# Kernel tuning notes

Measured on AMD Instinct MI355X. Metric: run time of the kernel, lower is better.

Reference implementation:

```python
import jax, jax.numpy as jnp
import numpy as np
from jax import lax

DIM = 64


def _dwconv(x, w, b):
    # x: [B,C,H,W], w: [C,1,kh,kw] depthwise, 'same' padding
    kh, kw = w.shape[2], w.shape[3]
    y = lax.conv_general_dilated(
        x, w, window_strides=(1, 1),
        padding=[(kh // 2, kh // 2), (kw // 2, kw // 2)],
        dimension_numbers=("NCHW", "OIHW", "NCHW"),
        feature_group_count=x.shape[1])
    return y + b[None, :, None, None]


def _conv1x1(x, w, b):
    y = lax.conv_general_dilated(
        x, w, window_strides=(1, 1), padding="VALID",
        dimension_numbers=("NCHW", "OIHW", "NCHW"))
    return y + b[None, :, None, None]


def _avgpool3(x):
    # PyTorch AvgPool2d(3,1,1) default count_include_pad=True -> sum/9
    s = lax.reduce_window(x, 0.0, lax.add, (1, 1, 3, 3), (1, 1, 1, 1),
                          [(0, 0), (0, 0), (1, 1), (1, 1)])
    return s / 9.0


def _maxpool3(x):
    return lax.reduce_window(x, -jnp.inf, lax.max, (1, 1, 3, 3), (1, 1, 1, 1),
                             [(0, 0), (0, 0), (1, 1), (1, 1)])


def setup_inputs() -> dict:
    key = jax.random.key(0)
    ks = jax.random.split(key, 18)
    C = DIM
    def w(k, shape):
        fan_in = shape[1] * shape[2] * shape[3]
        bound = 1.0 / np.sqrt(fan_in)
        return jax.random.uniform(k, shape, jnp.float32, -bound, bound)
    def b(k, fan_in):
        bound = 1.0 / np.sqrt(fan_in)
        return jax.random.uniform(k, (C,), jnp.float32, -bound, bound)
    return {
        "x": jax.random.normal(ks[0], (16, C, 128, 128), jnp.float32),
        "w55": w(ks[1], (C, 1, 5, 5)), "b55": b(ks[2], 25),
        "w17_0": w(ks[3], (C, 1, 1, 7)), "b17_0": b(ks[4], 7),
        "w17_1": w(ks[5], (C, 1, 7, 1)), "b17_1": b(ks[6], 7),
        "w111_0": w(ks[7], (C, 1, 1, 11)), "b111_0": b(ks[8], 11),
        "w111_1": w(ks[9], (C, 1, 11, 1)), "b111_1": b(ks[10], 11),
        "w211_0": w(ks[11], (C, 1, 1, 21)), "b211_0": b(ks[12], 21),
        "w211_1": w(ks[13], (C, 1, 21, 1)), "b211_1": b(ks[14], 21),
        "w11": w(ks[15], (C, C, 1, 1)), "b11": b(ks[16], C),
    }


def reference(x, w55, b55, w17_0, b17_0, w17_1, b17_1,
              w111_0, b111_0, w111_1, b111_1,
              w211_0, b211_0, w211_1, b211_1, w11, b11):
    def branch(inp):
        c55 = _dwconv(inp, w55, b55)
        c17 = _dwconv(_dwconv(inp, w17_0, b17_0), w17_1, b17_1)
        c111 = _dwconv(_dwconv(inp, w111_0, b111_0), w111_1, b111_1)
        c211 = _dwconv(_dwconv(inp, w211_0, b211_0), w211_1, b211_1)
        return _conv1x1(c55 + c17 + c111 + c211, w11, b11)

    mixer = branch(x)
    mixer_1 = branch(_avgpool3(x))
    mixer_2 = branch(_maxpool3(x))
    return (mixer + mixer_1 + mixer_2) * x
```

## Files before the change

kernel.cpp:

```cpp
#include <hip/hip_runtime.h>
#include <hip/hip_bf16.h>
#include <cstdint>

#define HH 128
#define WW 128
#define CC 64
#define BB 16
#define PLANE (HH*WW)
#define TPSTR 16512

#define XS_STR    52
#define XRAW_STR  60
#define XSTH_H    8736
#define H7_H      11328
#define UNION_F   7072
#define H11_H     14144
#define H21_H     16960
#define SMEM_FLOATS 9888

__device__ __forceinline__ float lo16(unsigned int u) {
  return __uint_as_float(u << 16);
}
__device__ __forceinline__ float hi16(unsigned int u) {
  return __uint_as_float(u & 0xffff0000u);
}

__device__ __forceinline__ void phase_a2_half(
    float* sm, __hip_bfloat16* hb, const float* xbuf, int tid, int tR0,
    int tC0, int rg_lo, int roff) {
  __hip_bfloat16* xsTh = hb + XSTH_H;
  for (int i = tid; i < 14 * 13; i += 256) {
    int rg = rg_lo + (i % 14);
    int jj = i / 14;
    int rr0 = rg * 3;
    const float* rp = xbuf + (rr0 - roff) * XRAW_STR + jj * 4;
    float w[5][8];
    #pragma unroll
    for (int k = 0; k < 5; ++k) {
      float4 a = *(const float4*)(rp + k * XRAW_STR);
      float4 b = *(const float4*)(rp + k * XRAW_STR + 4);
      w[k][0] = a.x; w[k][1] = a.y; w[k][2] = a.z; w[k][3] = a.w;
      w[k][4] = b.x; w[k][5] = b.y; w[k][6] = b.z; w[k][7] = b.w;
    }
    int gc0 = tC0 + jj * 4 - 12;
    bool cv[7];
    #pragma unroll
    for (int p = 1; p <= 6; ++p) cv[p] = (unsigned)(gc0 + p) < 128u;

    #pragma unroll
    for (int k = 0; k < 3; ++k) {
      int rr = rr0 + k;
      int gr = tR0 + rr - 10;
      bool rv0 = (unsigned)(gr - 1) < 128u;
      bool rv1 = (unsigned)(gr) < 128u;
      bool rv2 = (unsigned)(gr + 1) < 128u;
      float M0[7], M1[7], M2[7];
      #pragma unroll
      for (int p = 1; p <= 6; ++p) {
        M0[p] = (rv0 && cv[p]) ? w[k][p] : -3.402823466e38f;
        M1[p] = (rv1 && cv[p]) ? w[k + 1][p] : -3.402823466e38f;
        M2[p] = (rv2 && cv[p]) ? w[k + 2][p] : -3.402823466e38f;
      }
      float uq[4];
      #pragma unroll
      for (int q = 0; q < 4; ++q) {
        float s = w[k][q + 1] + w[k][q + 2] + w[k][q + 3] + w[k + 1][q + 1] +
                  w[k + 1][q + 2] + w[k + 1][q + 3] + w[k + 2][q + 1] +
                  w[k + 2][q + 2] + w[k + 2][q + 3];
        float m = fmaxf(
            fmaxf(fmaxf(M0[q + 1], M0[q + 2]), fmaxf(M0[q + 3], M1[q + 1])),
            fmaxf(fmaxf(M1[q + 2], M1[q + 3]),
                  fmaxf(fmaxf(M2[q + 1], M2[q + 2]), M2[q + 3])));
        float val = w[k + 1][q + 2] + s * (1.f / 9.f) + m;
        bool vo = rv1 && ((unsigned)(gc0 + q + 2) < 128u);
        uq[q] = vo ? val : 0.f;
      }
      *(float4*)(sm + rr * XS_STR + jj * 4) =
          make_float4(uq[0], uq[1], uq[2], uq[3]);
      int rt = rr - 8;
      if ((unsigned)rt < 68u) {
        #pragma unroll
        for (int q = 0; q < 4; ++q) {
          int ct = jj * 4 + q - 8;
          if ((unsigned)ct < 36u)
            xsTh[ct * 72 + rt] = __float2bfloat16(uq[q]);
        }
      }
    }
  }
}

__global__ __launch_bounds__(256, 4) void k_dwsum(
    const float* __restrict__ x, float* __restrict__ T,
    const float* __restrict__ w55, const float* __restrict__ b55,
    const float* __restrict__ w17_0, const float* __restrict__ b17_0,
    const float* __restrict__ w17_1, const float* __restrict__ b17_1,
    const float* __restrict__ w111_0, const float* __restrict__ b111_0,
    const float* __restrict__ w111_1, const float* __restrict__ b111_1,
    const float* __restrict__ w211_0, const float* __restrict__ b211_0,
    const float* __restrict__ w211_1, const float* __restrict__ b211_1) {
  __shared__ float sm[SMEM_FLOATS];
  __hip_bfloat16* hb = (__hip_bfloat16*)sm;

  const int bid = blockIdx.x;
  const int pl = bid >> 3;
  const int t = bid & 7;
  const int tR0 = (t >> 2) * 64;
  const int tC0 = (t & 3) * 32;
  const int ch = pl & (CC - 1);
  const float* xp = x + (size_t)pl * PLANE;
  float* Tp = T + (size_t)pl * TPSTR;
  const int tid = threadIdx.x;

  float* xbuf = sm + UNION_F;
  const int base_r = tR0 - 11, base_c = tC0 - 12;

  for (int i = tid; i < 44 * 14; i += 256) {
    int rr = i / 14;
    int jj = i - rr * 14;
    int gr = base_r + rr;
    int gc = base_c + jj * 4;
    float4 v = make_float4(0.f, 0.f, 0.f, 0.f);
    if ((unsigned)gr < 128u && (unsigned)gc < 128u)
      v = *(const float4*)(xp + gr * WW + gc);
    *(float4*)(xbuf + rr * XRAW_STR + jj * 4) = v;
  }
  __syncthreads();
  phase_a2_half(sm, hb, xbuf, tid, tR0, tC0, 0, 0);
  __syncthreads();
  for (int i = tid; i < 44 * 14; i += 256) {
    int rr = i / 14;
    int jj = i - rr * 14;
    int gr = base_r + 42 + rr;
    int gc = base_c + jj * 4;
    float4 v = make_float4(0.f, 0.f, 0.f, 0.f);
    if ((unsigned)gr < 128u && (unsigned)gc < 128u)
      v = *(const float4*)(xp + gr * WW + gc);
    *(float4*)(xbuf + rr * XRAW_STR + jj * 4) = v;
  }
  __syncthreads();
  phase_a2_half(sm, hb, xbuf, tid, tR0, tC0, 14, 42);

  float k7[7], k11[11], k21[21];
  #pragma unroll
  for (int i = 0; i < 7; ++i) k7[i] = w17_0[ch * 7 + i];
  #pragma unroll
  for (int i = 0; i < 11; ++i) k11[i] = w111_0[ch * 11 + i];
  #pragma unroll
  for (int i = 0; i < 21; ++i) k21[i] = w211_0[ch * 21 + i];
  float bb7 = 3.f * b17_0[ch];
  float bb11 = 3.f * b111_0[ch];
  float bb21 = 3.f * b211_0[ch];

  __syncthreads();

  for (int it = tid; it < 84 * 4; it += 256) {
    int rr = it % 84;
    int cg = it / 84;
    float w[28];
    const float* xr = sm + rr * XS_STR + cg * 8;
    #pragma unroll
    for (int j = 0; j < 7; ++j) {
      float4 v = *(const float4*)(xr + 4 * j);
      w[4 * j] = v.x; w[4 * j + 1] = v.y; w[4 * j + 2] = v.z; w[4 * j + 3] = v.w;
    }
    int gr = tR0 + rr - 10;
    bool rv = (unsigned)gr < 128u;
    bool v11r = (rr >= 5) && (rr <= 78);
    bool v7r = (rr >= 7) && (rr <= 76);
    #pragma unroll
    for (int j = 0; j < 8; ++j) {
      float a21 = bb21, a11 = bb11, a7 = bb7;
      #pragma unroll
      for (int d = 0; d < 21; ++d) a21 += k21[d] * w[j + d];
      #pragma unroll
      for (int d = 0; d < 11; ++d) a11 += k11[d] * w[j + 5 + d];
      #pragma unroll
      for (int d = 0; d < 7; ++d) a7 += k7[d] * w[j + 7 + d];
      int c = cg * 8 + j;
      hb[H21_H + c * 88 + rr] = __float2bfloat16(rv ? a21 : 0.f);
      if (v11r) hb[H11_H + c * 88 + rr - 5] = __float2bfloat16(rv ? a11 : 0.f);
      if (v7r) hb[H7_H + c * 88 + rr - 7] = __float2bfloat16(rv ? a7 : 0.f);
    }
  }

  float v7a[7], v11a[11], v21a[21], w5a[25];
  #pragma unroll
  for (int i = 0; i < 7; ++i) v7a[i] = w17_1[ch * 7 + i];
  #pragma unroll
  for (int i = 0; i < 11; ++i) v11a[i] = w111_1[ch * 11 + i];
  #pragma unroll
  for (int i = 0; i < 21; ++i) v21a[i] = w211_1[ch * 21 + i];
  #pragma unroll
  for (int i = 0; i < 25; ++i) w5a[i] = w55[ch * 25 + i];
  float bsum = 3.f * (b55[ch] + b17_1[ch] + b111_1[ch] + b211_1[ch]);

  __syncthreads();

  {
    int c = tid & 31;
    int r0 = (tid >> 5) * 8;
    float acc[8];
    #pragma unroll
    for (int j = 0; j < 8; ++j) acc[j] = bsum;

    float A[28];
    {
      const unsigned* p = (const unsigned*)&hb[H21_H + c * 88 + r0];
      uint4 q0 = *(const uint4*)p;
      uint4 q1 = *(const uint4*)(p + 4);
      uint4 q2 = *(const uint4*)(p + 8);
      uint2 q3 = *(const uint2*)(p + 12);
      A[0]=lo16(q0.x);A[1]=hi16(q0.x);A[2]=lo16(q0.y);A[3]=hi16(q0.y);
      A[4]=lo16(q0.z);A[5]=hi16(q0.z);A[6]=lo16(q0.w);A[7]=hi16(q0.w);
      A[8]=lo16(q1.x);A[9]=hi16(q1.x);A[10]=lo16(q1.y);A[11]=hi16(q1.y);
      A[12]=lo16(q1.z);A[13]=hi16(q1.z);A[14]=lo16(q1.w);A[15]=hi16(q1.w);
      A[16]=lo16(q2.x);A[17]=hi16(q2.x);A[18]=lo16(q2.y);A[19]=hi16(q2.y);
      A[20]=lo16(q2.z);A[21]=hi16(q2.z);A[22]=lo16(q2.w);A[23]=hi16(q2.w);
      A[24]=lo16(q3.x);A[25]=hi16(q3.x);A[26]=lo16(q3.y);A[27]=hi16(q3.y);
      #pragma unroll
      for (int d = 0; d < 21; ++d)
        #pragma unroll
        for (int j = 0; j < 8; ++j) acc[j] += v21a[d] * A[d + j];
    }
    {
      const unsigned* p = (const unsigned*)&hb[H11_H + c * 88 + r0];
      uint4 q0 = *(const uint4*)p;
      uint4 q1 = *(const uint4*)(p + 4);
      uint2 q2 = *(const uint2*)(p + 8);
      A[0]=lo16(q0.x);A[1]=hi16(q0.x);A[2]=lo16(q0.y);A[3]=hi16(q0.y);
      A[4]=lo16(q0.z);A[5]=hi16(q0.z);A[6]=lo16(q0.w);A[7]=hi16(q0.w);
      A[8]=lo16(q1.x);A[9]=hi16(q1.x);A[10]=lo16(q1.y);A[11]=hi16(q1.y);
      A[12]=lo16(q1.z);A[13]=hi16(q1.z);A[14]=lo16(q1.w);A[15]=hi16(q1.w);
      A[16]=lo16(q2.x);A[17]=hi16(q2.x);
      #pragma unroll
      for (int d = 0; d < 11; ++d)
        #pragma unroll
        for (int j = 0; j < 8; ++j) acc[j] += v11a[d] * A[d + j];
    }
    {
      const unsigned* p = (const unsigned*)&hb[H7_H + c * 88 + r0];
      uint4 q0 = *(const uint4*)p;
      uint4 q1 = *(const uint4*)(p + 4);
      A[0]=lo16(q0.x);A[1]=hi16(q0.x);A[2]=lo16(q0.y);A[3]=hi16(q0.y);
      A[4]=lo16(q0.z);A[5]=hi16(q0.z);A[6]=lo16(q0.w);A[7]=hi16(q0.w);
      A[8]=lo16(q1.x);A[9]=hi16(q1.x);A[10]=lo16(q1.y);A[11]=hi16(q1.y);
      A[12]=lo16(q1.z);A[13]=hi16(q1.z);
      #pragma unroll
      for (int d = 0; d < 7; ++d)
        #pragma unroll
        for (int j = 0; j < 8; ++j) acc[j] += v7a[d] * A[d + j];
    }
    {
      #pragma unroll
      for (int dc = 0; dc < 5; ++dc) {
        const unsigned* p = (const unsigned*)&hb[XSTH_H + (c + dc) * 72 + r0];
        uint4 q0 = *(const uint4*)p;
        uint2 q1 = *(const uint2*)(p + 4);
        float X[12];
        X[0]=lo16(q0.x);X[1]=hi16(q0.x);X[2]=lo16(q0.y);X[3]=hi16(q0.y);
        X[4]=lo16(q0.z);X[5]=hi16(q0.z);X[6]=lo16(q0.w);X[7]=hi16(q0.w);
        X[8]=lo16(q1.x);X[9]=hi16(q1.x);X[10]=lo16(q1.y);X[11]=hi16(q1.y);
        #pragma unroll
        for (int dr = 0; dr < 5; ++dr)
          #pragma unroll
          for (int j = 0; j < 8; ++j) acc[j] += w5a[dr * 5 + dc] * X[j + dr];
      }
    }
    #pragma unroll
    for (int j = 0; j < 8; ++j)
      Tp[(size_t)(tR0 + r0 + j) * WW + tC0 + c] = acc[j];
  }
}

__device__ __forceinline__ void gload_lds16(const float* g, float* l) {
  __builtin_amdgcn_global_load_lds(
      (const __attribute__((address_space(1))) void*)g,
      (__attribute__((address_space(3))) void*)l, 16, 0, 0);
}

__global__ __launch_bounds__(256, 4) void k_mix(const float* __restrict__ T,
                                                const float* __restrict__ x,
                                                const float* __restrict__ w11,
                                                const float* __restrict__ b11,
                                                float* __restrict__ out) {
  __shared__ float Tbuf[2][16 * 128];
  __shared__ float Wt[64 * 68];

  int bid = blockIdx.x;
  int b = bid >> 7;
  int px0 = (bid & 127) * 128;
  int tid = threadIdx.x;
  int lane = tid & 63;
  int wv = tid >> 6;

  const float* Tb = T + (size_t)b * 64 * TPSTR + px0;

  const int srow = wv * 4 + (lane >> 5);
  const int scol = (lane & 31) * 4;

  #pragma unroll
  for (int j = 0; j < 2; ++j)
    gload_lds16(Tb + (size_t)(srow + j * 2) * TPSTR + scol,
                &Tbuf[0][(wv * 4 + j * 2) * 128]);

  for (int i = tid; i < 4096; i += 256) {
    int co = i >> 6, ci = i & 63;
    Wt[ci * 68 + co] = w11[i];
  }

  int pxg = tid & 31;
  int cog = tid >> 5;
  const float* wp = Wt + cog * 8;

  const float* xb = x + (size_t)b * (CC * PLANE) + px0 + pxg * 4;
  float4 xv[8];
  #pragma unroll
  for (int a = 0; a < 8; ++a)
    xv[a] = *(const float4*)(xb + (size_t)(cog * 8 + a) * PLANE);

  float acc[8][4];
  #pragma unroll
  for (int a = 0; a < 8; ++a)
    #pragma unroll
    for (int p = 0; p < 4; ++p) acc[a][p] = 0.f;

  for (int q = 0; q < 4; ++q) {
    __syncthreads();
    if (q < 3) {
      #pragma unroll
      for (int j = 0; j < 2; ++j)
        gload_lds16(Tb + (size_t)((q + 1) * 16 + srow + j * 2) * TPSTR + scol,
                    &Tbuf[(q + 1) & 1][(wv * 4 + j * 2) * 128]);
    }
    const float* tp = Tbuf[q & 1] + pxg * 4;
    #pragma unroll
    for (int kk = 0; kk < 16; ++kk) {
      int k = q * 16 + kk;
      float4 tv = *(const float4*)(tp + kk * 128);
      float4 q0 = *(const float4*)(wp + k * 68);
      float4 q1 = *(const float4*)(wp + k * 68 + 4);
      float wf[8] = {q0.x, q0.y, q0.z, q0.w, q1.x, q1.y, q1.z, q1.w};
      float tvv[4] = {tv.x, tv.y, tv.z, tv.w};
      #pragma unroll
      for (int a = 0; a < 8; ++a)
        #pragma unroll
        for (int p = 0; p < 4; ++p) acc[a][p] += wf[a] * tvv[p];
    }
  }

  float* ob = out + (size_t)b * (CC * PLANE) + px0 + pxg * 4;
  #pragma unroll
  for (int a = 0; a < 8; ++a) {
    int co = cog * 8 + a;
    float bb = 3.f * b11[co];
    float4 o;
    o.x = (acc[a][0] + bb) * xv[a].x;
    o.y = (acc[a][1] + bb) * xv[a].y;
    o.z = (acc[a][2] + bb) * xv[a].z;
    o.w = (acc[a][3] + bb) * xv[a].w;
    *(float4*)(ob + (size_t)co * PLANE) = o;
  }
}

extern "C" void kernel_launch(void* const* d_in, const int* in_sizes, int n_in,
                              void* d_out, int out_size, void* d_ws,
                              size_t ws_size, hipStream_t stream) {
  const float* x = (const float*)d_in[0];
  const float* w55 = (const float*)d_in[1];
  const float* b55 = (const float*)d_in[2];
  const float* w17_0 = (const float*)d_in[3];
  const float* b17_0 = (const float*)d_in[4];
  const float* w17_1 = (const float*)d_in[5];
  const float* b17_1 = (const float*)d_in[6];
  const float* w111_0 = (const float*)d_in[7];
  const float* b111_0 = (const float*)d_in[8];
  const float* w111_1 = (const float*)d_in[9];
  const float* b111_1 = (const float*)d_in[10];
  const float* w211_0 = (const float*)d_in[11];
  const float* b211_0 = (const float*)d_in[12];
  const float* w211_1 = (const float*)d_in[13];
  const float* b211_1 = (const float*)d_in[14];
  const float* w11 = (const float*)d_in[15];
  const float* b11 = (const float*)d_in[16];
  float* outp = (float*)d_out;

  float* T = (float*)d_ws;

  k_dwsum<<<BB * CC * 8, 256, 0, stream>>>(
      x, T, w55, b55, w17_0, b17_0, w17_1, b17_1, w111_0, b111_0, w111_1,
      b111_1, w211_0, b211_0, w211_1, b211_1);
  k_mix<<<BB * 128, 256, 0, stream>>>(T, x, w11, b11, outp);
}
```

Before: 307.1 us.

## Load T directly into registers in k_mix instead of LDS staging

Rewrites the 1x1-conv mixing kernel so each thread handles one pixel and 32 output channels, reading its T column straight from global memory into registers with double-buffered register prefetch. This replaces the LDS double buffer filled by global_load_lds and its per-chunk barriers. Weights are now read as broadcast float4 rows from LDS. The x reads and output writes drop from float4 to scalar accesses, and register pressure rises from the 32 accumulators plus the prefetch buffers.

```diff
diff --git a/kernel.cpp b/kernel.cpp
--- a/kernel.cpp
+++ b/kernel.cpp
@@ -273,93 +273,78 @@
   }
 }
 
-__device__ __forceinline__ void gload_lds16(const float* g, float* l) {
-  __builtin_amdgcn_global_load_lds(
-      (const __attribute__((address_space(1))) void*)g,
-      (__attribute__((address_space(3))) void*)l, 16, 0, 0);
-}
-
 __global__ __launch_bounds__(256, 4) void k_mix(const float* __restrict__ T,
                                                 const float* __restrict__ x,
                                                 const float* __restrict__ w11,
                                                 const float* __restrict__ b11,
                                                 float* __restrict__ out) {
-  __shared__ float Tbuf[2][16 * 128];
   __shared__ float Wt[64 * 68];
 
   int bid = blockIdx.x;
   int b = bid >> 7;
   int px0 = (bid & 127) * 128;
   int tid = threadIdx.x;
-  int lane = tid & 63;
-  int wv = tid >> 6;
-
-  const float* Tb = T + (size_t)b * 64 * TPSTR + px0;
-
-  const int srow = wv * 4 + (lane >> 5);
-  const int scol = (lane & 31) * 4;
-
-  #pragma unroll
-  for (int j = 0; j < 2; ++j)
-    gload_lds16(Tb + (size_t)(srow + j * 2) * TPSTR + scol,
-                &Tbuf[0][(wv * 4 + j * 2) * 128]);
 
   for (int i = tid; i < 4096; i += 256) {
     int co = i >> 6, ci = i & 63;
     Wt[ci * 68 + co] = w11[i];
   }
 
-  int pxg = tid & 31;
-  int cog = tid >> 5;
-  const float* wp = Wt + cog * 8;
-
-  const float* xb = x + (size_t)b * (CC * PLANE) + px0 + pxg * 4;
-  float4 xv[8];
-  #pragma unroll
-  for (int a = 0; a < 8; ++a)
-    xv[a] = *(const float4*)(xb + (size_t)(cog * 8 + a) * PLANE);
-
-  float acc[8][4];
-  #pragma unroll
-  for (int a = 0; a < 8; ++a)
-    #pragma unroll
-    for (int p = 0; p < 4; ++p) acc[a][p] = 0.f;
-
-  for (int q = 0; q < 4; ++q) {
-    __syncthreads();
-    if (q < 3) {
-      #pragma unroll
-      for (int j = 0; j < 2; ++j)
-        gload_lds16(Tb + (size_t)((q + 1) * 16 + srow + j * 2) * TPSTR + scol,
-                    &Tbuf[(q + 1) & 1][(wv * 4 + j * 2) * 128]);
-    }
-    const float* tp = Tbuf[q & 1] + pxg * 4;
-    #pragma unroll
-    for (int kk = 0; kk < 16; ++kk) {
-      int k = q * 16 + kk;
-      float4 tv = *(const float4*)(tp + kk * 128);
-      float4 q0 = *(const float4*)(wp + k * 68);
-      float4 q1 = *(const float4*)(wp + k * 68 + 4);
-      float wf[8] = {q0.x, q0.y, q0.z, q0.w, q1.x, q1.y, q1.z, q1.w};
-      float tvv[4] = {tv.x, tv.y, tv.z, tv.w};
-      #pragma unroll
-      for (int a = 0; a < 8; ++a)
-        #pragma unroll
-        for (int p = 0; p < 4; ++p) acc[a][p] += wf[a] * tvv[p];
-    }
-  }
-
-  float* ob = out + (size_t)b * (CC * PLANE) + px0 + pxg * 4;
-  #pragma unroll
-  for (int a = 0; a < 8; ++a) {
-    int co = cog * 8 + a;
+  int px = tid & 127;
+  int coh = tid >> 7;
+  const float* Tb = T + (size_t)b * 64 * TPSTR + px0 + px;
+
+  float tb0[8], tb1[8];
+  #pragma unroll
+  for (int k = 0; k < 8; ++k) tb0[k] = Tb[(size_t)k * TPSTR];
+
+  __syncthreads();
+
+  float acc[32];
+  #pragma unroll
+  for (int a = 0; a < 32; ++a) acc[a] = 0.f;
+
+  const float* wbase = Wt + coh * 32;
+
+  #pragma unroll
+  for (int kc = 0; kc < 8; ++kc) {
+    float* cur = (kc & 1) ? tb1 : tb0;
+    float* nxt = (kc & 1) ? tb0 : tb1;
+    if (kc < 7) {
+      #pragma unroll
+      for (int k = 0; k < 8; ++k)
+        nxt[k] = Tb[(size_t)(kc * 8 + 8 + k) * TPSTR];
+    }
+    #pragma unroll
+    for (int kk = 0; kk < 8; ++kk) {
+      int ci = kc * 8 + kk;
+      const float* wr = wbase + ci * 68;
+      float4 w0 = *(const float4*)(wr);
+      float4 w1 = *(const float4*)(wr + 4);
+      float4 w2 = *(const float4*)(wr + 8);
+      float4 w3 = *(const float4*)(wr + 12);
+      float4 w4 = *(const float4*)(wr + 16);
+      float4 w5 = *(const float4*)(wr + 20);
+      float4 w6 = *(const float4*)(wr + 24);
+      float4 w7 = *(const float4*)(wr + 28);
+      float wf[32] = {w0.x, w0.y, w0.z, w0.w, w1.x, w1.y, w1.z, w1.w,
+                      w2.x, w2.y, w2.z, w2.w, w3.x, w3.y, w3.z, w3.w,
+                      w4.x, w4.y, w4.z, w4.w, w5.x, w5.y, w5.z, w5.w,
+                      w6.x, w6.y, w6.z, w6.w, w7.x, w7.y, w7.z, w7.w};
+      float tv = cur[kk];
+      #pragma unroll
+      for (int a = 0; a < 32; ++a) acc[a] += wf[a] * tv;
+    }
+  }
+
+  const float* xb = x + (size_t)b * (CC * PLANE) + px0 + px;
+  float* ob = out + (size_t)b * (CC * PLANE) + px0 + px;
+  #pragma unroll
+  for (int a = 0; a < 32; ++a) {
+    int co = coh * 32 + a;
     float bb = 3.f * b11[co];
-    float4 o;
-    o.x = (acc[a][0] + bb) * xv[a].x;
-    o.y = (acc[a][1] + bb) * xv[a].y;
-    o.z = (acc[a][2] + bb) * xv[a].z;
-    o.w = (acc[a][3] + bb) * xv[a].w;
-    *(float4*)(ob + (size_t)co * PLANE) = o;
+    float xv = xb[(size_t)co * PLANE];
+    ob[(size_t)co * PLANE] = (acc[a] + bb) * xv;
   }
 }
 
```

New measurement: 289.7 us. 1.06x faster.
